# Kernel tuning notes

Measured on AMD Instinct MI355X. Metric: run time of the kernel, lower is better.

## Reference

```python
import jax, jax.numpy as jnp
import numpy as np

B, T = 16384, 64
VOCAB, D, HD, FF = 10, 3, 4, 2
EPS = 1e-6


def _rms(x, w):
    return x * jax.lax.rsqrt(jnp.mean(x * x, axis=-1, keepdims=True) + EPS) * w


def _rope(x, theta=3.0):
    # x: [..., T, HD]; interleaved rotary, matching the torch RotaryEmbedding
    t = jnp.arange(x.shape[-2], dtype=x.dtype)
    inv_freq = 1.0 / theta ** (jnp.arange(0, HD, 2, dtype=x.dtype) / HD)  # [HD/2]
    freqs = jnp.outer(t, inv_freq)                                        # [T, HD/2]
    cos_f, sin_f = jnp.cos(freqs), jnp.sin(freqs)
    x1, x2 = x[..., ::2], x[..., 1::2]
    rot = jnp.stack([x1 * cos_f - x2 * sin_f, x1 * sin_f + x2 * cos_f], axis=-1)
    return rot.reshape(x.shape)


def setup_inputs() -> dict:
    key = jax.random.key(0)
    ks = jax.random.split(key, 12)
    f32 = jnp.float32
    return {
        "idx": jax.random.randint(ks[0], (B, T), 0, VOCAB, dtype=jnp.int32),
        "arc_A": jnp.asarray(2.5, f32),
        "arc_start": jnp.asarray(-1.2, f32),
        "arc_stride": jnp.asarray(0.29, f32),
        "w_ln1": jnp.ones((D,), f32) + 0.1 * jax.random.normal(ks[1], (D,), f32),
        "w_ln2": jnp.ones((D,), f32) + 0.1 * jax.random.normal(ks[2], (D,), f32),
        "w_lnf": jnp.ones((D,), f32) + 0.1 * jax.random.normal(ks[3], (D,), f32),
        "w_qn": jnp.ones((HD,), f32) + 0.1 * jax.random.normal(ks[4], (HD,), f32),
        "Wq": jax.random.normal(ks[5], (HD, D), f32) * 0.5,
        "Wk": jax.random.normal(ks[6], (HD, D), f32) * 0.5,
        "Wg": jax.random.normal(ks[7], (FF, D), f32) * 0.5,
        "Wu": jax.random.normal(ks[8], (FF, D), f32) * 0.5,
        "Wd": jax.random.normal(ks[9], (D, FF), f32) * 0.5,
    }


def reference(idx, arc_A, arc_start, arc_stride, w_ln1, w_ln2, w_lnf, w_qn,
              Wq, Wk, Wg, Wu, Wd):
    dt = arc_A.dtype
    # circular-arc token embedding table [VOCAB, 2]
    digits = jnp.arange(VOCAB, dtype=dt)
    angles = arc_start + digits * arc_stride
    table = jnp.stack([arc_A * jnp.cos(angles), arc_A * jnp.sin(angles)], axis=1)

    tok = table[idx]                                              # [B,T,2]
    pe = jnp.sin(jnp.arange(T, dtype=dt) * jnp.exp(jnp.asarray(-np.log(10000.0), dt)))
    pos = jnp.broadcast_to(pe[None, :, None], (idx.shape[0], T, 1))
    x = jnp.concatenate([tok, pos], axis=-1)                      # [B,T,3]

    h = _rms(x, w_ln1)
    q = _rms(h @ Wq.T, w_qn)                                      # [B,T,HD]
    k = _rms(h @ Wk.T, w_qn)
    v = h @ Wk.T                                                  # v = k pre-norm? no: v = k.clone() BEFORE q_norm
    q = _rope(q)
    k = _rope(k)

    scale = HD ** (-0.5)
    scores = jnp.einsum("btd,bsd->bts", q, k) * scale             # [B,T,T]
    causal = jnp.triu(jnp.ones((T, T), dtype=bool), k=1)
    scores = jnp.where(causal, -jnp.inf, scores)
    attn = jax.nn.softmax(scores, axis=-1)
    out = jnp.einsum("bts,bsd->btd", attn, v)                     # [B,T,HD]

    x = x + out @ Wq                                              # F.linear(out, Wq.T) == out @ Wq
    h = _rms(x, w_ln2)
    x = x + (jax.nn.silu(h @ Wg.T) * (h @ Wu.T)) @ Wd.T
    x = _rms(x, w_lnf)
    return x[..., :2] @ table.T                                   # [B,T,VOCAB]
```

## Files before the change

kernel.cpp:

```cpp
#include <hip/hip_runtime.h>
#include <math.h>


namespace {
constexpr int kVocab = 10;
constexpr float kEps = 1e-6f;
constexpr int kWaves = 4;

typedef __attribute__((ext_vector_type(8)))  short short8;
typedef __attribute__((ext_vector_type(16))) float float16;

constexpr int kOffQh  = 0;
constexpr int kOffQl  = 512;
constexpr int kOffKh  = 1024;
constexpr int kOffKl  = 1536;
constexpr int kOffP0  = 0;
constexpr int kOffP1  = 2560;
constexpr int kOffVt  = 7168;
constexpr int kOffO   = 0;
constexpr int kWaveLds = 8320;
constexpr int kP0P = 40;
constexpr int kP1P = 72;
constexpr int kVtP = 72;
constexpr int kOP  = 76;

__device__ __forceinline__ unsigned bf16_1(float a) {
    return (__float_as_uint(a) + 0x8000u) >> 16;
}
__device__ __forceinline__ unsigned pk_bf16(float a, float b) {
    const unsigned au = __float_as_uint(a) + 0x8000u;
    const unsigned bu = __float_as_uint(b) + 0x8000u;
    return (au >> 16) | (bu & 0xffff0000u);
}
__device__ __forceinline__ float bf_lo(unsigned u) { return __uint_as_float(u << 16); }
__device__ __forceinline__ float bf_hi(unsigned u) { return __uint_as_float(u & 0xffff0000u); }

__device__ __forceinline__ float16 mfma(short8 a, short8 b, float16 c) {
    return __builtin_amdgcn_mfma_f32_32x32x16_bf16(a, b, c, 0, 0, 0);
}

__device__ __forceinline__ short8 tok_frag(const char* wbase, int off, int tok, bool lo_half) {
    uint2 r = *(const uint2*)(wbase + off + tok * 8);
    uint4 t;
    t.x = lo_half ? r.x : 0u;
    t.y = lo_half ? r.y : 0u;
    t.z = 0u; t.w = 0u;
    return __builtin_bit_cast(short8, t);
}

template<bool MASKED>
__device__ __forceinline__ void exp_store(const float16& S, ushort* rowbase, int h, int m) {
#pragma unroll
    for (int c = 0; c < 4; ++c) {
        float e[4];
#pragma unroll
        for (int j = 0; j < 4; ++j) {
            float sc = S[4 * c + j];
            if (MASKED) sc = ((j + 8 * c) <= m) ? sc : -INFINITY;
            e[j] = __builtin_amdgcn_exp2f(sc);
        }
        uint2 w;
        w.x = pk_bf16(e[0], e[1]);
        w.y = pk_bf16(e[2], e[3]);
        *(uint2*)(rowbase + 8 * c + 4 * h) = w;
    }
}

__global__ __launch_bounds__(256, 4) void adder_model_kernel(
    const int* __restrict__ idx,
    const float* __restrict__ p_arcA,
    const float* __restrict__ p_arcStart,
    const float* __restrict__ p_arcStride,
    const float* __restrict__ w_ln1,
    const float* __restrict__ w_ln2,
    const float* __restrict__ w_lnf,
    const float* __restrict__ w_qn,
    const float* __restrict__ Wq,
    const float* __restrict__ Wk,
    const float* __restrict__ Wg,
    const float* __restrict__ Wu,
    const float* __restrict__ Wd,
    float* __restrict__ out)
{
    __shared__ __align__(16) char smem[kWaves][kWaveLds];
    __shared__ __align__(16) float table_s[kVocab * 2];

    const int lane = threadIdx.x & 63;
    const int wid  = threadIdx.x >> 6;
    char* wbase = &smem[wid][0];

    if (threadIdx.x < kVocab) {
        const float ang = p_arcStart[0] + (float)threadIdx.x * p_arcStride[0];
        const float A = p_arcA[0];
        table_s[2 * threadIdx.x]     = A * __cosf(ang);
        table_s[2 * threadIdx.x + 1] = A * __sinf(ang);
    }
    __syncthreads();

    const float t_f = (float)lane;
    const float pe  = __sinf(t_f * 1e-4f);
    const float c0  = __cosf(t_f);
    const float s0  = __sinf(t_f);
    const float ang1 = t_f * 0.57735026918962576f;
    const float c1  = __cosf(ang1);
    const float s1  = __sinf(ang1);

    const float wl1_0 = w_ln1[0], wl1_1 = w_ln1[1], wl1_2 = w_ln1[2];
    const float wl2_0 = w_ln2[0], wl2_1 = w_ln2[1], wl2_2 = w_ln2[2];
    const float wlf0 = w_lnf[0], wlf1 = w_lnf[1];
    const float wqn0 = w_qn[0], wqn1 = w_qn[1], wqn2 = w_qn[2], wqn3 = w_qn[3];
    const float Wq00 = Wq[0],  Wq01 = Wq[1],  Wq02 = Wq[2];
    const float Wq10 = Wq[3],  Wq11 = Wq[4],  Wq12 = Wq[5];
    const float Wq20 = Wq[6],  Wq21 = Wq[7],  Wq22 = Wq[8];
    const float Wq30 = Wq[9],  Wq31 = Wq[10], Wq32 = Wq[11];
    const float Wk00 = Wk[0],  Wk01 = Wk[1],  Wk02 = Wk[2];
    const float Wk10 = Wk[3],  Wk11 = Wk[4],  Wk12 = Wk[5];
    const float Wk20 = Wk[6],  Wk21 = Wk[7],  Wk22 = Wk[8];
    const float Wk30 = Wk[9],  Wk31 = Wk[10], Wk32 = Wk[11];
    const float Wg00 = Wg[0],  Wg01 = Wg[1],  Wg02 = Wg[2];
    const float Wg10 = Wg[3],  Wg11 = Wg[4],  Wg12 = Wg[5];
    const float Wu00 = Wu[0],  Wu01 = Wu[1],  Wu02 = Wu[2];
    const float Wu10 = Wu[3],  Wu11 = Wu[4],  Wu12 = Wu[5];
    const float Wd00 = Wd[0],  Wd01 = Wd[1];
    const float Wd10 = Wd[2],  Wd11 = Wd[3];
    const float Wd20 = Wd[4],  Wd21 = Wd[5];

    const int row = (int)blockIdx.x * kWaves + wid;

    const int tix = idx[(size_t)row * 64 + lane];
    const float2 emb = *(const float2*)(table_s + 2 * tix);
    const float x0i = emb.x, x1i = emb.y, x2i = pe;

    const float r1 = __builtin_amdgcn_rsqf((x0i*x0i + x1i*x1i + x2i*x2i) * (1.0f/3.0f) + kEps);
    const float h0 = x0i * r1 * wl1_0;
    const float h1 = x1i * r1 * wl1_1;
    const float h2 = x2i * r1 * wl1_2;

    const float qp0 = h0*Wq00 + h1*Wq01 + h2*Wq02;
    const float qp1 = h0*Wq10 + h1*Wq11 + h2*Wq12;
    const float qp2 = h0*Wq20 + h1*Wq21 + h2*Wq22;
    const float qp3 = h0*Wq30 + h1*Wq31 + h2*Wq32;
    const float v0 = h0*Wk00 + h1*Wk01 + h2*Wk02;
    const float v1 = h0*Wk10 + h1*Wk11 + h2*Wk12;
    const float v2 = h0*Wk20 + h1*Wk21 + h2*Wk22;
    const float v3 = h0*Wk30 + h1*Wk31 + h2*Wk32;

    const float rq = __builtin_amdgcn_rsqf((qp0*qp0 + qp1*qp1 + qp2*qp2 + qp3*qp3) * 0.25f + kEps);
    const float rk = __builtin_amdgcn_rsqf((v0*v0 + v1*v1 + v2*v2 + v3*v3) * 0.25f + kEps);
    const float qn0 = qp0*rq*wqn0, qn1 = qp1*rq*wqn1, qn2 = qp2*rq*wqn2, qn3 = qp3*rq*wqn3;
    const float kn0 = v0*rk*wqn0,  kn1 = v1*rk*wqn1,  kn2 = v2*rk*wqn2,  kn3 = v3*rk*wqn3;

    constexpr float kQS = 0.72134752044448170f;
    const float q0 = (qn0*c0 - qn1*s0) * kQS;
    const float q1 = (qn0*s0 + qn1*c0) * kQS;
    const float q2 = (qn2*c1 - qn3*s1) * kQS;
    const float q3 = (qn2*s1 + qn3*c1) * kQS;
    const float k0 = kn0*c0 - kn1*s0;
    const float k1 = kn0*s0 + kn1*c0;
    const float k2 = kn2*c1 - kn3*s1;
    const float k3 = kn2*s1 + kn3*c1;

    uint2 qh, ql, kh, kl;
    qh.x = pk_bf16(q0, q1); qh.y = pk_bf16(q2, q3);
    ql.x = pk_bf16(q0 - bf_lo(qh.x), q1 - bf_hi(qh.x));
    ql.y = pk_bf16(q2 - bf_lo(qh.y), q3 - bf_hi(qh.y));
    kh.x = pk_bf16(k0, k1); kh.y = pk_bf16(k2, k3);
    kl.x = pk_bf16(k0 - bf_lo(kh.x), k1 - bf_hi(kh.x));
    kl.y = pk_bf16(k2 - bf_lo(kh.y), k3 - bf_hi(kh.y));
    *(uint2*)(wbase + kOffQh + lane * 8) = qh;
    *(uint2*)(wbase + kOffQl + lane * 8) = ql;
    *(uint2*)(wbase + kOffKh + lane * 8) = kh;
    *(uint2*)(wbase + kOffKl + lane * 8) = kl;

    ushort* Vt = (ushort*)(wbase + kOffVt);
    Vt[0 * kVtP + lane] = (ushort)bf16_1(v0);
    Vt[1 * kVtP + lane] = (ushort)bf16_1(v1);
    Vt[2 * kVtP + lane] = (ushort)bf16_1(v2);
    Vt[3 * kVtP + lane] = (ushort)bf16_1(v3);
    Vt[4 * kVtP + lane] = (ushort)0x3F80;
    __threadfence_block();

    const int  tloc = lane & 31;
    const bool loh  = lane < 32;
    const int  h    = lane >> 5;
    const int  m    = tloc - 4 * h;

    const short8 aKh0 = tok_frag(wbase, kOffKh, tloc,      loh);
    const short8 aKl0 = tok_frag(wbase, kOffKl, tloc,      loh);
    const short8 aKh1 = tok_frag(wbase, kOffKh, tloc + 32, loh);
    const short8 aKl1 = tok_frag(wbase, kOffKl, tloc + 32, loh);
    const short8 bQh0 = tok_frag(wbase, kOffQh, tloc,      loh);
    const short8 bQl0 = tok_frag(wbase, kOffQl, tloc,      loh);
    const short8 bQh1 = tok_frag(wbase, kOffQh, tloc + 32, loh);
    const short8 bQl1 = tok_frag(wbase, kOffQl, tloc + 32, loh);
    __threadfence_block();

    float16 Z = {0,0,0,0,0,0,0,0,0,0,0,0,0,0,0,0};
    float16 S00 = mfma(aKl0, bQh0, mfma(aKh0, bQl0, mfma(aKh0, bQh0, Z)));
    float16 S01 = mfma(aKl0, bQh1, mfma(aKh0, bQl1, mfma(aKh0, bQh1, Z)));
    float16 S11 = mfma(aKl1, bQh1, mfma(aKh1, bQl1, mfma(aKh1, bQh1, Z)));

    ushort* P0 = (ushort*)(wbase + kOffP0);
    ushort* P1 = (ushort*)(wbase + kOffP1);
    exp_store<true >(S00, P0 + tloc * kP0P,      h, m);
    exp_store<false>(S01, P1 + tloc * kP1P,      h, m);
    exp_store<true >(S11, P1 + tloc * kP1P + 32, h, m);
    __threadfence_block();

    short8 vb[4];
#pragma unroll
    for (int kc = 0; kc < 4; ++kc)
        vb[kc] = __builtin_bit_cast(short8,
            *(const uint4*)(Vt + (tloc & 7) * kVtP + 16 * kc + 8 * h));

    float16 acc0 = Z, acc1 = Z;
#pragma unroll
    for (int kc = 0; kc < 2; ++kc) {
        short8 pa = __builtin_bit_cast(short8,
            *(const uint4*)(P0 + tloc * kP0P + 16 * kc + 8 * h));
        acc0 = mfma(pa, vb[kc], acc0);
    }
#pragma unroll
    for (int kc = 0; kc < 4; ++kc) {
        short8 pa = __builtin_bit_cast(short8,
            *(const uint4*)(P1 + tloc * kP1P + 16 * kc + 8 * h));
        acc1 = mfma(pa, vb[kc], acc1);
    }

    float* Ol = (float*)(wbase + kOffO);
    if (tloc < 5) {
#pragma unroll
        for (int c = 0; c < 4; ++c) {
            float4 w0 = make_float4(acc0[4*c], acc0[4*c+1], acc0[4*c+2], acc0[4*c+3]);
            *(float4*)(Ol + tloc * kOP +      8 * c + 4 * h) = w0;
            float4 w1 = make_float4(acc1[4*c], acc1[4*c+1], acc1[4*c+2], acc1[4*c+3]);
            *(float4*)(Ol + tloc * kOP + 32 + 8 * c + 4 * h) = w1;
        }
    }
    __threadfence_block();

    const float o0r = Ol[0 * kOP + lane];
    const float o1r = Ol[1 * kOP + lane];
    const float o2r = Ol[2 * kOP + lane];
    const float o3r = Ol[3 * kOP + lane];
    const float lr  = Ol[4 * kOP + lane];

    const float invl = __builtin_amdgcn_rcpf(lr);
    const float o0 = o0r * invl, o1 = o1r * invl, o2 = o2r * invl, o3 = o3r * invl;

    const float xa0 = x0i + o0*Wq00 + o1*Wq10 + o2*Wq20 + o3*Wq30;
    const float xa1 = x1i + o0*Wq01 + o1*Wq11 + o2*Wq21 + o3*Wq31;
    const float xa2 = x2i + o0*Wq02 + o1*Wq12 + o2*Wq22 + o3*Wq32;

    const float r2 = __builtin_amdgcn_rsqf((xa0*xa0 + xa1*xa1 + xa2*xa2) * (1.0f/3.0f) + kEps);
    const float hh0 = xa0*r2*wl2_0, hh1 = xa1*r2*wl2_1, hh2 = xa2*r2*wl2_2;
    const float g0 = hh0*Wg00 + hh1*Wg01 + hh2*Wg02;
    const float g1 = hh0*Wg10 + hh1*Wg11 + hh2*Wg12;
    const float u0 = hh0*Wu00 + hh1*Wu01 + hh2*Wu02;
    const float u1 = hh0*Wu10 + hh1*Wu11 + hh2*Wu12;
    constexpr float kL2E = 1.4426950408889634f;
    const float f0 = g0 * __builtin_amdgcn_rcpf(1.0f + __builtin_amdgcn_exp2f(-g0 * kL2E)) * u0;
    const float f1 = g1 * __builtin_amdgcn_rcpf(1.0f + __builtin_amdgcn_exp2f(-g1 * kL2E)) * u1;
    const float xf0 = xa0 + f0*Wd00 + f1*Wd01;
    const float xf1 = xa1 + f0*Wd10 + f1*Wd11;
    const float xf2 = xa2 + f0*Wd20 + f1*Wd21;

    const float rf = __builtin_amdgcn_rsqf((xf0*xf0 + xf1*xf1 + xf2*xf2) * (1.0f/3.0f) + kEps);
    const float y0 = xf0 * rf * wlf0;
    const float y1 = xf1 * rf * wlf1;

    const float4* tb4 = (const float4*)table_s;
    const float4 T0 = tb4[0], T1 = tb4[1], T2 = tb4[2], T3 = tb4[3], T4 = tb4[4];

    float2* op = (float2*)(out + (size_t)(row * 64 + lane) * kVocab);
    op[0] = float2{y0*T0.x + y1*T0.y, y0*T0.z + y1*T0.w};
    op[1] = float2{y0*T1.x + y1*T1.y, y0*T1.z + y1*T1.w};
    op[2] = float2{y0*T2.x + y1*T2.y, y0*T2.z + y1*T2.w};
    op[3] = float2{y0*T3.x + y1*T3.y, y0*T3.z + y1*T3.w};
    op[4] = float2{y0*T4.x + y1*T4.y, y0*T4.z + y1*T4.w};
}
}

extern "C" void kernel_launch(void* const* d_in, const int* in_sizes, int n_in,
                              void* d_out, int out_size, void* d_ws, size_t ws_size,
                              hipStream_t stream) {
    (void)in_sizes; (void)n_in; (void)d_ws; (void)ws_size; (void)out_size;
    const int*   idx       = (const int*)  d_in[0];
    const float* arcA      = (const float*)d_in[1];
    const float* arcStart  = (const float*)d_in[2];
    const float* arcStride = (const float*)d_in[3];
    const float* w_ln1     = (const float*)d_in[4];
    const float* w_ln2     = (const float*)d_in[5];
    const float* w_lnf     = (const float*)d_in[6];
    const float* w_qn      = (const float*)d_in[7];
    const float* Wq        = (const float*)d_in[8];
    const float* Wk        = (const float*)d_in[9];
    const float* Wg        = (const float*)d_in[10];
    const float* Wu        = (const float*)d_in[11];
    const float* Wd        = (const float*)d_in[12];
    float* out = (float*)d_out;

    dim3 grid(4096), block(256);
    hipLaunchKernelGGL(adder_model_kernel, grid, block, 0, stream,
                       idx, arcA, arcStart, arcStride,
                       w_ln1, w_ln2, w_lnf, w_qn, Wq, Wk, Wg, Wu, Wd, out);
}
```

Baseline: 109.4 us.

## Feed softmax probabilities to PV MFMA from registers instead of LDS

Exponentiated scores are packed into bf16 registers and passed directly as A operands to the PV MFMAs, rather than being written to LDS and read back. To make the register layout of the score accumulator line up with the MFMA input layout, the V columns are stored into LDS with a bit permutation of the lane index. This removes the P round trip through LDS and one fence, and shrinks per-wave LDS, which could allow more waves per CU. The risk is that the permutation or the operand ordering is wrong, which would silently corrupt results, and register pressure goes up.

```diff
diff --git a/kernel.cpp b/kernel.cpp
--- a/kernel.cpp
+++ b/kernel.cpp
@@ -14,13 +14,9 @@
 constexpr int kOffQl  = 512;
 constexpr int kOffKh  = 1024;
 constexpr int kOffKl  = 1536;
-constexpr int kOffP0  = 0;
-constexpr int kOffP1  = 2560;
-constexpr int kOffVt  = 7168;
-constexpr int kOffO   = 0;
-constexpr int kWaveLds = 8320;
-constexpr int kP0P = 40;
-constexpr int kP1P = 72;
+constexpr int kOffVt  = 2048;
+constexpr int kOffO   = 3200;
+constexpr int kWaveLds = 4736;
 constexpr int kVtP = 72;
 constexpr int kOP  = 76;
 
@@ -49,21 +45,26 @@
 }
 
 template<bool MASKED>
-__device__ __forceinline__ void exp_store(const float16& S, ushort* rowbase, int h, int m) {
+__device__ __forceinline__ void exp_pack(const float16& S, unsigned* out, int m) {
 #pragma unroll
-    for (int c = 0; c < 4; ++c) {
-        float e[4];
-#pragma unroll
-        for (int j = 0; j < 4; ++j) {
-            float sc = S[4 * c + j];
-            if (MASKED) sc = ((j + 8 * c) <= m) ? sc : -INFINITY;
-            e[j] = __builtin_amdgcn_exp2f(sc);
+    for (int i = 0; i < 8; ++i) {
+        const int r0 = 2 * i, r1 = 2 * i + 1;
+        float sa = S[r0], sb = S[r1];
+        if (MASKED) {
+            sa = (((r0 & 3) + 8 * (r0 >> 2)) <= m) ? sa : -INFINITY;
+            sb = (((r1 & 3) + 8 * (r1 >> 2)) <= m) ? sb : -INFINITY;
         }
-        uint2 w;
-        w.x = pk_bf16(e[0], e[1]);
-        w.y = pk_bf16(e[2], e[3]);
-        *(uint2*)(rowbase + 8 * c + 4 * h) = w;
+        out[i] = pk_bf16(__builtin_amdgcn_exp2f(sa), __builtin_amdgcn_exp2f(sb));
     }
+}
+
+__device__ __forceinline__ short8 af(const unsigned* p) {
+    uint4 t;
+    t.x = p[0]; t.y = p[1]; t.z = p[2]; t.w = p[3];
+    return __builtin_bit_cast(short8, t);
+}
+__device__ __forceinline__ short8 ld8(const void* p) {
+    return __builtin_bit_cast(short8, *(const uint4*)p);
 }
 
 __global__ __launch_bounds__(256, 4) void adder_model_kernel(
@@ -173,11 +174,12 @@
     *(uint2*)(wbase + kOffKl + lane * 8) = kl;
 
     ushort* Vt = (ushort*)(wbase + kOffVt);
-    Vt[0 * kVtP + lane] = (ushort)bf16_1(v0);
-    Vt[1 * kVtP + lane] = (ushort)bf16_1(v1);
-    Vt[2 * kVtP + lane] = (ushort)bf16_1(v2);
-    Vt[3 * kVtP + lane] = (ushort)bf16_1(v3);
-    Vt[4 * kVtP + lane] = (ushort)0x3F80;
+    const int vcol = (lane & ~12) | ((lane & 4) << 1) | ((lane & 8) >> 1);
+    Vt[0 * kVtP + vcol] = (ushort)bf16_1(v0);
+    Vt[1 * kVtP + vcol] = (ushort)bf16_1(v1);
+    Vt[2 * kVtP + vcol] = (ushort)bf16_1(v2);
+    Vt[3 * kVtP + vcol] = (ushort)bf16_1(v3);
+    Vt[4 * kVtP + vcol] = (ushort)0x3F80;
     __threadfence_block();
 
     const int  tloc = lane & 31;
@@ -193,39 +195,27 @@
     const short8 bQl0 = tok_frag(wbase, kOffQl, tloc,      loh);
     const short8 bQh1 = tok_frag(wbase, kOffQh, tloc + 32, loh);
     const short8 bQl1 = tok_frag(wbase, kOffQl, tloc + 32, loh);
-    __threadfence_block();
+
+    short8 vb[4];
+#pragma unroll
+    for (int kc = 0; kc < 4; ++kc)
+        vb[kc] = ld8(Vt + (tloc & 7) * kVtP + 16 * kc + 8 * h);
 
     float16 Z = {0,0,0,0,0,0,0,0,0,0,0,0,0,0,0,0};
     float16 S00 = mfma(aKl0, bQh0, mfma(aKh0, bQl0, mfma(aKh0, bQh0, Z)));
     float16 S01 = mfma(aKl0, bQh1, mfma(aKh0, bQl1, mfma(aKh0, bQh1, Z)));
     float16 S11 = mfma(aKl1, bQh1, mfma(aKh1, bQl1, mfma(aKh1, bQh1, Z)));
 
-    ushort* P0 = (ushort*)(wbase + kOffP0);
-    ushort* P1 = (ushort*)(wbase + kOffP1);
-    exp_store<true >(S00, P0 + tloc * kP0P,      h, m);
-    exp_store<false>(S01, P1 + tloc * kP1P,      h, m);
-    exp_store<true >(S11, P1 + tloc * kP1P + 32, h, m);
-    __threadfence_block();
-
-    short8 vb[4];
-#pragma unroll
-    for (int kc = 0; kc < 4; ++kc)
-        vb[kc] = __builtin_bit_cast(short8,
-            *(const uint4*)(Vt + (tloc & 7) * kVtP + 16 * kc + 8 * h));
-
-    float16 acc0 = Z, acc1 = Z;
-#pragma unroll
-    for (int kc = 0; kc < 2; ++kc) {
-        short8 pa = __builtin_bit_cast(short8,
-            *(const uint4*)(P0 + tloc * kP0P + 16 * kc + 8 * h));
-        acc0 = mfma(pa, vb[kc], acc0);
-    }
-#pragma unroll
-    for (int kc = 0; kc < 4; ++kc) {
-        short8 pa = __builtin_bit_cast(short8,
-            *(const uint4*)(P1 + tloc * kP1P + 16 * kc + 8 * h));
-        acc1 = mfma(pa, vb[kc], acc1);
-    }
+    unsigned p00[8], p01[8], p11[8];
+    exp_pack<true >(S00, p00, m);
+    exp_pack<false>(S01, p01, m);
+    exp_pack<true >(S11, p11, m);
+
+    float16 acc0 = mfma(af(p00 + 4), vb[1], mfma(af(p00), vb[0], Z));
+    float16 acc1 = mfma(af(p11 + 4), vb[3],
+                   mfma(af(p11),     vb[2],
+                   mfma(af(p01 + 4), vb[1],
+                   mfma(af(p01),     vb[0], Z))));
 
     float* Ol = (float*)(wbase + kOffO);
     if (tloc < 5) {
```

New measurement: 106.3 us. 1.03x faster.
